# Kernel optimization log

Measured on AMD Instinct MI355X. Metric: run time of the kernel, lower is better.

Reference implementation:

```python
import jax, jax.numpy as jnp
import numpy as np

LOG2PI = 1.8378770664093453  # log(2*pi)


def _pixel_positions(d, h, w):
    # centered coordinates, stacked as (x, y, z) per the torch module
    z = jnp.arange(d, dtype=jnp.float32) - (d - 1) / 2.0
    y = jnp.arange(h, dtype=jnp.float32) - (h - 1) / 2.0
    x = jnp.arange(w, dtype=jnp.float32) - (w - 1) / 2.0
    zz = jnp.broadcast_to(z[:, None, None], (d, h, w))
    yy = jnp.broadcast_to(y[None, :, None], (d, h, w))
    xx = jnp.broadcast_to(x[None, None, :], (d, h, w))
    return jnp.stack([xx, yy, zz], axis=-1).reshape(-1, 3)  # (N, 3)


def setup_inputs() -> dict:
    key = jax.random.key(0)
    k0, k1, k2, k3, k4 = jax.random.split(key, 5)
    B, D = 512, 256
    d, h, w = 16, 64, 64
    scale = 1.0 / np.sqrt(D)
    return {
        "representation": jax.random.normal(k0, (B, D), dtype=jnp.float32),
        "mean_w": jax.random.normal(k1, (3, D), dtype=jnp.float32) * scale,
        "mean_b": jax.random.normal(k2, (3,), dtype=jnp.float32) * 0.1,
        "scale_w": jax.random.normal(k3, (6, D), dtype=jnp.float32) * scale,
        "scale_b": jax.random.normal(k4, (6,), dtype=jnp.float32) * 0.1,
        "pixel_positions": _pixel_positions(d, h, w),
    }


def reference(representation, mean_w, mean_b, scale_w, scale_b, pixel_positions):
    # linear heads
    means = representation @ mean_w.T + mean_b            # (B, 3)
    s_raw = representation @ scale_w.T + scale_b          # (B, 6)
    s = jax.nn.elu(s_raw) + 1.0                           # (B, 6)

    # FillScaleTriL with SoftplusTransform on the diagonal.
    # tril_indices(3,3) row-major order: (0,0),(1,0),(1,1),(2,0),(2,1),(2,2)
    l00 = jax.nn.softplus(s[:, 0])
    l10 = s[:, 1]
    l11 = jax.nn.softplus(s[:, 2])
    l20 = s[:, 3]
    l21 = s[:, 4]
    l22 = jax.nn.softplus(s[:, 5])

    # Mahalanobis term via analytic forward-substitution of L z = (x - mu)
    diff = pixel_positions[None, :, :] - means[:, None, :]  # (B, N, 3)
    z0 = diff[..., 0] / l00[:, None]
    z1 = (diff[..., 1] - l10[:, None] * z0) / l11[:, None]
    z2 = (diff[..., 2] - l20[:, None] * z0 - l21[:, None] * z1) / l22[:, None]
    maha = z0 * z0 + z1 * z1 + z2 * z2                     # (B, N)

    log_det = jnp.log(l00) + jnp.log(l11) + jnp.log(l22)   # (B,)
    log_probs = -0.5 * maha - 1.5 * LOG2PI - log_det[:, None]  # (B, N)

    # stable normalize over the pixel grid (matches torch code incl. eps)
    lp = log_probs - jnp.max(log_probs, axis=1, keepdims=True)
    p = jnp.exp(lp)
    return p / (jnp.sum(p, axis=1, keepdims=True) + 1e-10)
```

## Files before the change

kernel.cpp:

```cpp
#include <hip/hip_runtime.h>
#include <math.h>


#define HL2E 0.7213475204444817f
#define L2E  1.4426950408889634f

__device__ __forceinline__ float waveSum(float v) {
#pragma unroll
    for (int off = 32; off; off >>= 1) v += __shfl_xor(v, off, 64);
    return v;
}

__global__ __launch_bounds__(1024, 8)
void mvn_profile_kernel(const float* __restrict__ rep,
                        const float* __restrict__ mean_w,
                        const float* __restrict__ mean_b,
                        const float* __restrict__ scale_w,
                        const float* __restrict__ scale_b,
                        float* __restrict__ out)
{
    const int b    = blockIdx.x;
    const int tid  = threadIdx.x;
    const int lane = tid & 63;
    const int wave = tid >> 6;

    __shared__ float s_dots[9];
    __shared__ float s_params[10];
    __shared__ float s_red[16];
    __shared__ float s_bcast;

    if (wave < 9) {
        const float4* r4 = (const float4*)(rep + (size_t)b * 256);
        const float*  wrow = (wave < 3) ? (mean_w + wave * 256)
                                        : (scale_w + (wave - 3) * 256);
        const float4* w4 = (const float4*)wrow;
        float4 a = r4[lane];
        float4 w = w4[lane];
        float d = a.x * w.x + a.y * w.y + a.z * w.z + a.w * w.w;
        d = waveSum(d);
        if (lane == 0) s_dots[wave] = d;
    }
    __syncthreads();

    if (tid == 0) {
        float mx = s_dots[0] + mean_b[0];
        float my = s_dots[1] + mean_b[1];
        float mz = s_dots[2] + mean_b[2];
        float s[6];
#pragma unroll
        for (int j = 0; j < 6; j++) {
            float x = s_dots[3 + j] + scale_b[j];
            s[j] = (x > 0.0f) ? (x + 1.0f) : (expm1f(x) + 1.0f);
        }
        float l00 = fmaxf(s[0], 0.0f) + log1pf(expf(-fabsf(s[0])));
        float l10 = s[1];
        float l11 = fmaxf(s[2], 0.0f) + log1pf(expf(-fabsf(s[2])));
        float l20 = s[3];
        float l21 = s[4];
        float l22 = fmaxf(s[5], 0.0f) + log1pf(expf(-fabsf(s[5])));
        float i00 = 1.0f / l00, i11 = 1.0f / l11, i22 = 1.0f / l22;

        float gx = fminf(fmaxf(roundf(mx + 31.5f), 0.0f), 63.0f) - 31.5f;
        float z0 = (gx - mx) * i00;
        float ty = my + l10 * z0;
        float gy = fminf(fmaxf(roundf(ty + 31.5f), 0.0f), 63.0f) - 31.5f;
        float z1 = ((gy - my) - l10 * z0) * i11;
        float tz = mz + l20 * z0 + l21 * z1;
        float gz = fminf(fmaxf(roundf(tz + 7.5f), 0.0f), 15.0f) - 7.5f;
        float z2 = ((gz - mz) - l20 * z0 - l21 * z1) * i22;
        float mahag = z0 * z0 + z1 * z1 + z2 * z2;

        s_params[0] = mx;  s_params[1] = my;  s_params[2] = mz;
        s_params[3] = i00; s_params[4] = l10; s_params[5] = i11;
        s_params[6] = l20; s_params[7] = l21; s_params[8] = i22;
        s_params[9] = HL2E * mahag;
    }
    __syncthreads();

    const float mx  = s_params[0], my  = s_params[1], mz  = s_params[2];
    const float i00 = s_params[3], l10 = s_params[4], i11 = s_params[5];
    const float l20 = s_params[6], l21 = s_params[7], i22 = s_params[8];
    const float sc2 = s_params[9];

    const float py = (float)(tid >> 4) - 31.5f;
    const float dy = py - my;

    float cc2[4];
    float e2[4];
#pragma unroll
    for (int j = 0; j < 4; j++) {
        float px = (float)(((tid * 4) & 63) + j) - 31.5f;
        float dx = px - mx;
        float z0 = dx * i00;
        float z1 = (dy - l10 * z0) * i11;
        e2[j]  = (mz + l20 * z0 + l21 * z1) * i22;
        cc2[j] = sc2 - HL2E * (z0 * z0 + z1 * z1);
    }

    float tsum = 0.0f;
#pragma unroll
    for (int k = 0; k < 16; k++) {
        float t = ((float)k - 7.5f) * i22;
#pragma unroll
        for (int j = 0; j < 4; j++) {
            float z2 = t - e2[j];
            float q  = fmaf(z2 * z2, -HL2E, cc2[j]);
            tsum += exp2f(q);
        }
    }
    tsum = waveSum(tsum);
    if (lane == 0) s_red[wave] = tsum;
    __syncthreads();
    if (wave == 0) {
        float v = (lane < 16) ? s_red[lane] : 0.0f;
        v = waveSum(v);
        if (lane == 0) s_bcast = 1.0f / (v + 1e-10f);
    }
    __syncthreads();
    const float r = s_bcast;

    float* orow = out + (size_t)b * 65536 + (size_t)tid * 4;
#pragma unroll
    for (int k = 0; k < 16; k++) {
        float t = ((float)k - 7.5f) * i22;
        float4 o;
        {
            float z2 = t - e2[0];
            o.x = exp2f(fmaf(z2 * z2, -HL2E, cc2[0])) * r;
        }
        {
            float z2 = t - e2[1];
            o.y = exp2f(fmaf(z2 * z2, -HL2E, cc2[1])) * r;
        }
        {
            float z2 = t - e2[2];
            o.z = exp2f(fmaf(z2 * z2, -HL2E, cc2[2])) * r;
        }
        {
            float z2 = t - e2[3];
            o.w = exp2f(fmaf(z2 * z2, -HL2E, cc2[3])) * r;
        }
        *(float4*)(orow + (size_t)k * 4096) = o;
    }
}

extern "C" void kernel_launch(void* const* d_in, const int* in_sizes, int n_in,
                              void* d_out, int out_size, void* d_ws, size_t ws_size,
                              hipStream_t stream) {
    const float* rep     = (const float*)d_in[0];
    const float* mean_w  = (const float*)d_in[1];
    const float* mean_b  = (const float*)d_in[2];
    const float* scale_w = (const float*)d_in[3];
    const float* scale_b = (const float*)d_in[4];
    float* out = (float*)d_out;

    const int B = in_sizes[0] / 256;
    hipLaunchKernelGGL(mvn_profile_kernel, dim3(B), dim3(1024), 0, stream,
                       rep, mean_w, mean_b, scale_w, scale_b, out);
}
```

Before: 167.7 us.

## Split into params/sum kernel and wide output kernel via workspace

Splits the fused per-batch kernel into two launches. The first computes the linear heads, the Cholesky parameters and the normalizing sum with 256 threads per batch, then writes them to a workspace. The second spreads the output writes across 8 blocks per batch so more blocks write concurrently. This trades a second launch and recomputing every exponential for higher parallelism on the write-bound output phase. It also switches to the native exp2 intrinsic.

```diff
diff --git a/kernel.cpp b/kernel.cpp
--- a/kernel.cpp
+++ b/kernel.cpp
@@ -3,7 +3,6 @@
 
 
 #define HL2E 0.7213475204444817f
-#define L2E  1.4426950408889634f
 
 __device__ __forceinline__ float waveSum(float v) {
 #pragma unroll
@@ -11,13 +10,13 @@
     return v;
 }
 
-__global__ __launch_bounds__(1024, 8)
-void mvn_profile_kernel(const float* __restrict__ rep,
-                        const float* __restrict__ mean_w,
-                        const float* __restrict__ mean_b,
-                        const float* __restrict__ scale_w,
-                        const float* __restrict__ scale_b,
-                        float* __restrict__ out)
+__global__ __launch_bounds__(256)
+void mvn_params_kernel(const float* __restrict__ rep,
+                       const float* __restrict__ mean_w,
+                       const float* __restrict__ mean_b,
+                       const float* __restrict__ scale_w,
+                       const float* __restrict__ scale_b,
+                       float* __restrict__ ws)
 {
     const int b    = blockIdx.x;
     const int tid  = threadIdx.x;
@@ -26,19 +25,19 @@
 
     __shared__ float s_dots[9];
     __shared__ float s_params[10];
-    __shared__ float s_red[16];
-    __shared__ float s_bcast;
+    __shared__ float s_red[4];
 
-    if (wave < 9) {
+    {
         const float4* r4 = (const float4*)(rep + (size_t)b * 256);
-        const float*  wrow = (wave < 3) ? (mean_w + wave * 256)
-                                        : (scale_w + (wave - 3) * 256);
-        const float4* w4 = (const float4*)wrow;
         float4 a = r4[lane];
-        float4 w = w4[lane];
-        float d = a.x * w.x + a.y * w.y + a.z * w.z + a.w * w.w;
-        d = waveSum(d);
-        if (lane == 0) s_dots[wave] = d;
+        for (int r = wave; r < 9; r += 4) {
+            const float* wrow = (r < 3) ? (mean_w + r * 256)
+                                        : (scale_w + (r - 3) * 256);
+            float4 w = ((const float4*)wrow)[lane];
+            float d = a.x * w.x + a.y * w.y + a.z * w.z + a.w * w.w;
+            d = waveSum(d);
+            if (lane == 0) s_dots[r] = d;
+        }
     }
     __syncthreads();
 
@@ -82,65 +81,87 @@
     const float l20 = s_params[6], l21 = s_params[7], i22 = s_params[8];
     const float sc2 = s_params[9];
 
-    const float py = (float)(tid >> 4) - 31.5f;
-    const float dy = py - my;
-
-    float cc2[4];
-    float e2[4];
-#pragma unroll
-    for (int j = 0; j < 4; j++) {
-        float px = (float)(((tid * 4) & 63) + j) - 31.5f;
-        float dx = px - mx;
-        float z0 = dx * i00;
-        float z1 = (dy - l10 * z0) * i11;
-        e2[j]  = (mz + l20 * z0 + l21 * z1) * i22;
-        cc2[j] = sc2 - HL2E * (z0 * z0 + z1 * z1);
-    }
+    const float px  = (float)(tid & 63) - 31.5f;
+    const float z0  = (px - mx) * i00;
+    const float m10 = my + l10 * z0;
+    const float m20 = mz + l20 * z0;
+    const float cc0 = fmaf(z0 * z0, -HL2E, sc2);
 
     float tsum = 0.0f;
-#pragma unroll
-    for (int k = 0; k < 16; k++) {
-        float t = ((float)k - 7.5f) * i22;
-#pragma unroll
-        for (int j = 0; j < 4; j++) {
-            float z2 = t - e2[j];
-            float q  = fmaf(z2 * z2, -HL2E, cc2[j]);
-            tsum += exp2f(q);
-        }
+#pragma unroll 8
+    for (int i = 0; i < 256; i++) {
+        int yz = 4 * i + wave;
+        float py = (float)(yz & 63) - 31.5f;
+        float pz = (float)(yz >> 6) - 7.5f;
+        float z1 = (py - m10) * i11;
+        float c2 = fmaf(l21, z1, m20);
+        float z2 = (pz - c2) * i22;
+        float ssq = fmaf(z2, z2, z1 * z1);
+        float q = fmaf(ssq, -HL2E, cc0);
+        tsum += __builtin_amdgcn_exp2f(q);
     }
     tsum = waveSum(tsum);
     if (lane == 0) s_red[wave] = tsum;
     __syncthreads();
-    if (wave == 0) {
-        float v = (lane < 16) ? s_red[lane] : 0.0f;
-        v = waveSum(v);
-        if (lane == 0) s_bcast = 1.0f / (v + 1e-10f);
+
+    if (tid == 0) {
+        float tot = s_red[0] + s_red[1] + s_red[2] + s_red[3];
+        float* p = ws + (size_t)b * 16;
+#pragma unroll
+        for (int j = 0; j < 10; j++) p[j] = s_params[j];
+        p[10] = 1.0f / (tot + 1e-10f);
     }
-    __syncthreads();
-    const float r = s_bcast;
+}
 
-    float* orow = out + (size_t)b * 65536 + (size_t)tid * 4;
+__global__ __launch_bounds__(256)
+void mvn_out_kernel(const float* __restrict__ ws,
+                    float* __restrict__ out)
+{
+    const int blk = blockIdx.x;
+    const int b   = blk >> 3;
+    const int c   = blk & 7;
+    const int tid = threadIdx.x;
+
+    const float* p = ws + (size_t)b * 16;
+    const float mx  = p[0], my  = p[1], mz  = p[2];
+    const float i00 = p[3], l10 = p[4], i11 = p[5];
+    const float l20 = p[6], l21 = p[7], i22 = p[8];
+    const float sc2 = p[9], r = p[10];
+
+    float z0v[4], m10v[4], m20v[4], cc0v[4];
 #pragma unroll
-    for (int k = 0; k < 16; k++) {
-        float t = ((float)k - 7.5f) * i22;
+    for (int j = 0; j < 4; j++) {
+        float px = (float)(((tid * 4) & 63) + j) - 31.5f;
+        float z0 = (px - mx) * i00;
+        z0v[j]  = z0;
+        m10v[j] = my + l10 * z0;
+        m20v[j] = mz + l20 * z0;
+        cc0v[j] = fmaf(z0 * z0, -HL2E, sc2);
+    }
+    (void)z0v;
+
+    const int n0     = c * 8192 + tid * 4;
+    const int yzbase = c * 128 + (tid >> 4);
+    float* orow = out + (size_t)b * 65536 + n0;
+
+#pragma unroll
+    for (int k = 0; k < 8; k++) {
+        int yz = yzbase + k * 16;
+        float py = (float)(yz & 63) - 31.5f;
+        float pz = (float)(yz >> 6) - 7.5f;
+        float vv[4];
+#pragma unroll
+        for (int j = 0; j < 4; j++) {
+            float z1  = (py - m10v[j]) * i11;
+            float c2  = fmaf(l21, z1, m20v[j]);
+            float z2  = (pz - c2) * i22;
+            float ssq = fmaf(z2, z2, z1 * z1);
+            float q   = fmaf(ssq, -HL2E, cc0v[j]);
+            vv[j] = __builtin_amdgcn_exp2f(q) * r;
+        }
         float4 o;
-        {
-            float z2 = t - e2[0];
-            o.x = exp2f(fmaf(z2 * z2, -HL2E, cc2[0])) * r;
-        }
-        {
-            float z2 = t - e2[1];
-            o.y = exp2f(fmaf(z2 * z2, -HL2E, cc2[1])) * r;
-        }
-        {
-            float z2 = t - e2[2];
-            o.z = exp2f(fmaf(z2 * z2, -HL2E, cc2[2])) * r;
-        }
-        {
-            float z2 = t - e2[3];
-            o.w = exp2f(fmaf(z2 * z2, -HL2E, cc2[3])) * r;
-        }
-        *(float4*)(orow + (size_t)k * 4096) = o;
+        o.x = vv[0]; o.y = vv[1]; o.z = vv[2]; o.w = vv[3];
+        *(float4*)(orow + (size_t)k * 1024) = o;
     }
 }
 
@@ -153,8 +174,11 @@
     const float* scale_w = (const float*)d_in[3];
     const float* scale_b = (const float*)d_in[4];
     float* out = (float*)d_out;
+    float* ws  = (float*)d_ws;
 
     const int B = in_sizes[0] / 256;
-    hipLaunchKernelGGL(mvn_profile_kernel, dim3(B), dim3(1024), 0, stream,
-                       rep, mean_w, mean_b, scale_w, scale_b, out);
+    hipLaunchKernelGGL(mvn_params_kernel, dim3(B), dim3(256), 0, stream,
+                       rep, mean_w, mean_b, scale_w, scale_b, ws);
+    hipLaunchKernelGGL(mvn_out_kernel, dim3(B * 8), dim3(256), 0, stream,
+                       ws, out);
 }
```

Result: no change. 164.4 us (-1.9%).
